# Kernel optimization log

Measured on AMD Instinct MI355X. Metric: run time of the kernel, lower is better.

Reference implementation:

```python
import jax, jax.numpy as jnp
import numpy as np

B, TQ, M, D, H, F, L = 4, 512, 512, 1024, 16, 4096, 6
S = D // H
R = TQ + M  # relative-attention length = memory + query
CUTOFFS = [20000, 40000, 200000]
PROJ_FACTOR = 4
LN_EPS = 1e-6
NEG_INF = -1e9


def setup_inputs() -> dict:
    key = jax.random.key(0)
    ks = iter(jax.random.split(key, 64))

    def w(shape, scale=0.02):
        return jax.random.normal(next(ks), shape, jnp.float32) * scale

    inp = {}
    inp['token_ids'] = jax.random.randint(next(ks), (B, TQ), 0, CUTOFFS[-1])
    inp['memories'] = w((L, B, M, D))
    starts = [0] + CUTOFFS
    pf = 1
    for i in range(len(CUTOFFS)):
        psize = max(1, D // pf)
        inp['emb_table%d' % i] = w((starts[i + 1] - starts[i], psize))
        inp['emb_proj%d' % i] = w((psize, D))
        pf *= PROJ_FACTOR
    inp['wq'] = w((L, D, H, S)); inp['wk'] = w((L, D, H, S))
    inp['wv'] = w((L, D, H, S)); inp['wr'] = w((L, D, H, S))
    inp['wo'] = w((L, H, S, D))
    inp['content_bias'] = w((L, H, S)); inp['position_bias'] = w((L, H, S))
    inp['ln1_scale'] = jnp.ones((L, D)); inp['ln1_bias'] = jnp.zeros((L, D))
    inp['ln2_scale'] = jnp.ones((L, D)); inp['ln2_bias'] = jnp.zeros((L, D))
    inp['ffn_w1'] = w((L, D, F)); inp['ffn_b1'] = jnp.zeros((L, F))
    inp['ffn_w2'] = w((L, F, D)); inp['ffn_b2'] = jnp.zeros((L, D))
    return inp


def layernorm(x, scale, bias):
    mu = jnp.mean(x, axis=-1, keepdims=True)
    var = jnp.var(x, axis=-1, keepdims=True)
    return (x - mu) * jax.lax.rsqrt(var + LN_EPS) * scale + bias


def rel_shift(x):
    # x: [B, H, Q, R] -> shifted so position j aligns with relative distance
    b, h, q, r = x.shape
    x = jnp.pad(x, ((0, 0), (0, 0), (0, 0), (1, 0)))
    x = x.reshape(b, h, r + 1, q)[:, :, 1:, :]
    return x.reshape(b, h, q, r)


def positional_encoding(r_len, d):
    pos = jnp.arange(r_len - 1, -1, -1, dtype=jnp.float32)  # r_len-1 ... 0
    inv_freq = 1.0 / (10000.0 ** (jnp.arange(0, d, 2, dtype=jnp.float32) / d))
    sinusoid = pos[:, None] * inv_freq[None, :]
    return jnp.concatenate([jnp.sin(sinusoid), jnp.cos(sinusoid)], axis=-1)


def adaptive_embed(ids, tables, projs):
    # jit-friendly version of AdaptiveEmbedding.compute_embeddings:
    # gather per-cluster, project up to D, combine via masks.
    d = projs[0].shape[-1]
    y = jnp.zeros(ids.shape + (d,), jnp.float32)
    starts = [0] + CUTOFFS
    for tab, proj, lo, hi in zip(tables, projs, starts[:-1], starts[1:]):
        mask = (ids >= lo) & (ids < hi)
        idx = jnp.clip(ids - lo, 0, tab.shape[0] - 1)
        emb = jnp.einsum('btp,pd->btd', tab[idx], proj)
        y = y + jnp.where(mask[..., None], emb, 0.0)
    return y * (d ** 0.5)


def transformer_xl(token_ids, memories, emb_tables, emb_projs, wq, wk, wv, wr,
                   wo, content_bias, position_bias, ln1_scale, ln1_bias,
                   ln2_scale, ln2_bias, ffn_w1, ffn_b1, ffn_w2, ffn_b2):
    x = adaptive_embed(token_ids, emb_tables, emb_projs)  # [B, TQ, D]
    pe = positional_encoding(R, D)                        # [R, D]
    q_idx = jnp.arange(TQ)[:, None]
    r_idx = jnp.arange(R)[None, :]
    future = r_idx > q_idx + M                            # [TQ, R], True=masked
    scale = 1.0 / np.sqrt(S).astype(np.float32)
    for l in range(L):
        q = jnp.einsum('btd,dhs->bths', x, wq[l])
        kv_in = jnp.concatenate([memories[l], x], axis=1)  # [B, R, D]
        k = jnp.einsum('brd,dhs->brhs', kv_in, wk[l])
        v = jnp.einsum('brd,dhs->brhs', kv_in, wv[l])
        r = jnp.einsum('rd,dhs->rhs', pe, wr[l])
        ac = jnp.einsum('bqhs,brhs->bhqr', q + content_bias[l], k)
        bd = rel_shift(jnp.einsum('bqhs,rhs->bhqr', q + position_bias[l], r))
        scores = (ac + bd) * scale
        scores = jnp.where(future[None, None], NEG_INF, scores)
        attn = jax.nn.softmax(scores, axis=-1)
        ctx = jnp.einsum('bhqr,brhs->bqhs', attn, v)
        out = jnp.einsum('bqhs,hsd->bqd', ctx, wo[l])
        x = layernorm(x + out, ln1_scale[l], ln1_bias[l])
        h = jax.nn.relu(jnp.einsum('btd,df->btf', x, ffn_w1[l]) + ffn_b1[l])
        h = jnp.einsum('btf,fd->btd', h, ffn_w2[l]) + ffn_b2[l]
        x = layernorm(x + h, ln2_scale[l], ln2_bias[l])
    return x


def reference(token_ids, memories, emb_table0, emb_proj0, emb_table1,
              emb_proj1, emb_table2, emb_proj2, wq, wk, wv, wr, wo,
              content_bias, position_bias, ln1_scale, ln1_bias, ln2_scale,
              ln2_bias, ffn_w1, ffn_b1, ffn_w2, ffn_b2):
    return transformer_xl(
        token_ids, memories,
        [emb_table0, emb_table1, emb_table2],
        [emb_proj0, emb_proj1, emb_proj2],
        wq, wk, wv, wr, wo, content_bias, position_bias,
        ln1_scale, ln1_bias, ln2_scale, ln2_bias,
        ffn_w1, ffn_b1, ffn_w2, ffn_b2)
```

## Files before the change

### kernel.cpp

```cpp
#include <hip/hip_runtime.h>


#define Bc 4
#define TQc 512
#define Mc 512
#define Dc 1024
#define Hc 16
#define Sc 64
#define Fc 4096
#define Lc 6
#define Rc 1024
#define KCAT 1344
#define DDc ((size_t)Dc * Dc)
#define NEG_INF_F (-1e9f)

typedef unsigned short ushortT;
typedef __attribute__((ext_vector_type(8))) short bfrag;
typedef __attribute__((ext_vector_type(4))) float facc;

__device__ inline ushortT f2bf(float f) {
    unsigned int u = __builtin_bit_cast(unsigned int, f);
    u = (u + 0x7FFFu + ((u >> 16) & 1u)) >> 16;
    return (ushortT)u;
}

#define CP16(gp, lp)                                                        \
    __builtin_amdgcn_global_load_lds(                                       \
        (const __attribute__((address_space(1))) unsigned int*)(gp),        \
        (__attribute__((address_space(3))) unsigned int*)(lp), 16, 0, 0)

__device__ inline bfrag lds_frag(const ushortT* lds, int row, int cg) {
    int c = cg ^ (row & 7);
    return *reinterpret_cast<const bfrag*>(
        reinterpret_cast<const char*>(lds) + row * 128 + c * 16);
}

template<int BM, int BN, int OUTM, bool BIAS, bool RELU, bool DUALQ,
         bool KVSRC = false, bool KVOUT = false>
__global__ __launch_bounds__(256) void mgemm(
    const ushortT* __restrict__ A, const ushortT* __restrict__ A2,
    const ushortT* __restrict__ Bt,
    const float* __restrict__ bias, const float* __restrict__ bias2,
    float* __restrict__ Cf, ushortT* __restrict__ Cb, ushortT* __restrict__ Cb2,
    int K, int lda, int ldb, int ldc,
    long long sA1, long long sB1, long long sC1, float oscale) {
    constexpr int WTM = BM / 2, WTN = BN / 2;
    constexpr int FM = WTM / 16, FN = WTN / 16;
    __shared__ ushortT sA[2][BM * 64];
    __shared__ ushortT sB[2][BN * 64];
    int tid = threadIdx.x;
    int wave = tid >> 6, lane = tid & 63;
    int r16 = lane & 15, kgrp = lane >> 4;
    int wr = wave >> 1, wc = wave & 1;
    int z = blockIdx.z;
    A  += (long long)z * sA1;
    Bt += (long long)z * sB1;
    long long coff = (long long)z * sC1;
    if (OUTM != 1) Cf += coff;
    if (OUTM != 0 || DUALQ) Cb += coff;

    int row0 = blockIdx.y * BM, col0 = blockIdx.x * BN;
    facc acc[FM][FN] = {};

    auto STAGE = [&](int buf, int k0) {
        #pragma unroll
        for (int it = 0; it < BM / 32; ++it) {
            int s = it * 256 + tid;
            int row = s >> 3, c = s & 7;
            int cs = c ^ (row & 7);
            const char* g;
            if constexpr (KVSRC) {
                int arow = row0 + row;
                int bq = arow >> 10;
                int r = arow & 1023;
                if (r < Mc)
                    g = (const char*)(A + ((size_t)bq * Mc + r) * lda + k0) + cs * 16;
                else
                    g = (const char*)(A2 + ((size_t)bq * TQc + (r - Mc)) * lda + k0) + cs * 16;
            } else {
                g = (const char*)(A + (size_t)(row0 + row) * lda + k0) + cs * 16;
            }
            CP16(g, (char*)sA[buf] + s * 16);
        }
        #pragma unroll
        for (int it = 0; it < BN / 32; ++it) {
            int s = it * 256 + tid;
            int row = s >> 3, c = s & 7;
            int cs = c ^ (row & 7);
            CP16((const char*)(Bt + (size_t)(col0 + row) * ldb + k0) + cs * 16,
                 (char*)sB[buf] + s * 16);
        }
    };

    STAGE(0, 0);
    __syncthreads();
    int nk = K >> 6;
    for (int t = 0; t < nk; ++t) {
        int cur = t & 1;
        if (t + 1 < nk) STAGE(cur ^ 1, (t + 1) << 6);
        #pragma unroll
        for (int ks = 0; ks < 2; ++ks) {
            bfrag af[FM], bf[FN];
            #pragma unroll
            for (int mi = 0; mi < FM; ++mi)
                af[mi] = lds_frag(sA[cur], wr * WTM + mi * 16 + r16, ks * 4 + kgrp);
            #pragma unroll
            for (int ni = 0; ni < FN; ++ni)
                bf[ni] = lds_frag(sB[cur], wc * WTN + ni * 16 + r16, ks * 4 + kgrp);
            #pragma unroll
            for (int mi = 0; mi < FM; ++mi)
                #pragma unroll
                for (int ni = 0; ni < FN; ++ni)
                    acc[mi][ni] = __builtin_amdgcn_mfma_f32_16x16x32_bf16(
                        af[mi], bf[ni], acc[mi][ni], 0, 0, 0);
        }
        __syncthreads();
    }

    if constexpr (KVOUT) {
        if (col0 >= 1024) {
            ushortT* sT = (ushortT*)sA;
            int b = row0 >> 10, r0l = row0 & 1023;
            int h0 = (col0 - 1024) >> 6;
            #pragma unroll
            for (int p = 0; p < 2; ++p) {
                __syncthreads();
                if (wc == p) {
                    #pragma unroll
                    for (int mi = 0; mi < FM; ++mi)
                        #pragma unroll
                        for (int ni = 0; ni < FN; ++ni) {
                            int srow = ni * 16 + r16;
                            int cbase = wr * 64 + mi * 16 + kgrp * 4;
                            short4 s4;
                            s4.x = (short)f2bf(acc[mi][ni][0]);
                            s4.y = (short)f2bf(acc[mi][ni][1]);
                            s4.z = (short)f2bf(acc[mi][ni][2]);
                            s4.w = (short)f2bf(acc[mi][ni][3]);
                            *(short4*)(sT + srow * 132 + cbase) = s4;
                        }
                }
                __syncthreads();
                int h = h0 + p;
                #pragma unroll
                for (int it = 0; it < 4; ++it) {
                    int srow = it * 16 + (tid >> 4);
                    int rch = (tid & 15) * 8;
                    short4 lo = *(short4*)(sT + srow * 132 + rch);
                    short4 hi = *(short4*)(sT + srow * 132 + rch + 4);
                    ushortT* dst = Cb2 + ((size_t)((b * 16 + h) * 64 + srow)) * Rc
                                   + r0l + rch;
                    *(short4*)dst = lo;
                    *(short4*)(dst + 4) = hi;
                }
            }
            return;
        }
    }

    #pragma unroll
    for (int mi = 0; mi < FM; ++mi) {
        #pragma unroll
        for (int ni = 0; ni < FN; ++ni) {
            int gcol = col0 + wc * WTN + ni * 16 + r16;
            float bv = 0.0f, bv2 = 0.0f;
            if (BIAS || DUALQ) bv = bias[gcol];
            if (DUALQ) bv2 = bias2[gcol];
            #pragma unroll
            for (int j = 0; j < 4; ++j) {
                int grow = row0 + wr * WTM + mi * 16 + kgrp * 4 + j;
                float v = acc[mi][ni][j];
                if constexpr (DUALQ) {
                    Cb [(size_t)grow * ldc + gcol] = f2bf((v + bv) * oscale);
                    Cb2[(size_t)grow * ldc + gcol] = f2bf((v + bv2) * oscale);
                } else if constexpr (OUTM == 2) {
                    v *= oscale;
                    Cf[(size_t)grow * ldc + gcol] = v;
                    Cb[(size_t)grow * ldc + gcol] = f2bf(v);
                } else {
                    if (BIAS) v += bv;
                    if (RELU) v = fmaxf(v, 0.0f);
                    if constexpr (OUTM == 0)
                        Cf[(size_t)grow * ldc + gcol] = v;
                    else
                        Cb[(size_t)grow * ldc + gcol] = f2bf(v);
                }
            }
        }
    }
}

__global__ __launch_bounds__(256) void fused_attn(
    const ushortT* __restrict__ qc, const ushortT* __restrict__ qp,
    const ushortT* __restrict__ kb, const ushortT* __restrict__ vT,
    const ushortT* __restrict__ rp, ushortT* __restrict__ ctx) {
    int n_id = (int)(blockIdx.y << 3) | (int)blockIdx.x;
    int b0 = n_id & 1, b7 = (n_id >> 7) & 1, b8 = (n_id >> 8) & 1;
    int u = (b7 << 1) | b0;
    int qt = (b0 ^ b8) ? (7 - u) : u;
    int bh = (n_id >> 1) & 63;
    int b = bh >> 4, h = bh & 15;
    int q0 = qt * 64;
    __shared__ __align__(16) char smem[73728];
    ushortT* sQc = (ushortT*)smem;
    ushortT* sQp = (ushortT*)(smem + 8192);
    float*   sBD = (float*)smem;
    ushortT* sK  = (ushortT*)(smem + 16384);
    ushortT* sV  = (ushortT*)(smem + 32768);
    ushortT* sR  = (ushortT*)(smem + 49152);
    int tid = threadIdx.x;
    int lane = tid & 63, wq = tid >> 6;
    int r16 = lane & 15, kgrp = lane >> 4;
    char* sPb = smem + wq * 4096;

    const ushortT* qcb = qc + (size_t)(b * TQc + q0) * Dc + h * 64;
    const ushortT* qpb = qp + (size_t)(b * TQc + q0) * Dc + h * 64;
    const ushortT* kbb = kb + (size_t)b * Rc * 1024 + h * 64;
    const ushortT* vTb = vT + (size_t)bh * 64 * Rc;
    const ushortT* rpb = rp + h * 64;
    int rrbase0 = 448 - q0;
    int iters = qt + 9;

    #pragma unroll
    for (int it = 0; it < 2; ++it) {
        int s = it * 256 + tid;
        int row = s >> 3, c = s & 7;
        int cs = c ^ (row & 7);
        CP16((const char*)(qcb + (size_t)row * Dc) + cs * 16, (char*)sQc + s * 16);
        CP16((const char*)(qpb + (size_t)row * Dc) + cs * 16, (char*)sQp + s * 16);
        CP16((const char*)(kbb + (size_t)row * 1024) + cs * 16, (char*)sK + s * 16);
        CP16((const char*)(vTb + (size_t)row * Rc) + cs * 16, (char*)sV + s * 16);
    }
    #pragma unroll
    for (int hR = 0; hR < 2; ++hR) {
        #pragma unroll
        for (int it = 0; it < 2; ++it) {
            int s = it * 256 + tid;
            int row = s >> 3, c = s & 7;
            int cs = c ^ (row & 7);
            int gr = rrbase0 + hR * 64 + row;
            gr = gr > 1023 ? 1023 : gr;
            CP16((const char*)(rpb + (size_t)gr * Dc) + cs * 16,
                 (char*)sR + hR * 8192 + s * 16);
        }
    }
    __syncthreads();

    bfrag hqc[2], hqp[2];
    #pragma unroll
    for (int ks = 0; ks < 2; ++ks) {
        hqc[ks] = lds_frag(sQc, wq * 16 + r16, ks * 4 + kgrp);
        hqp[ks] = lds_frag(sQp, wq * 16 + r16, ks * 4 + kgrp);
    }
    __syncthreads();

    facc accO[4] = {};
    float m[4] = {-1e30f, -1e30f, -1e30f, -1e30f};
    float lsum[4] = {};

    for (int itj = 0; itj < iters; ++itj) {
        int j0 = itj * 64;
        __syncthreads();
        int cur = itj & 1;
        int ph0 = itj % 3, ph1 = (itj + 1) % 3;

        if (itj + 1 < iters) {
            int jn = j0 + 64;
            #pragma unroll
            for (int it2 = 0; it2 < 2; ++it2) {
                int s = it2 * 256 + tid;
                int row = s >> 3, c = s & 7;
                int cs = c ^ (row & 7);
                CP16((const char*)(kbb + (size_t)(jn + row) * 1024) + cs * 16,
                     (char*)sK + (cur ^ 1) * 8192 + s * 16);
                CP16((const char*)(vTb + (size_t)row * Rc + jn) + cs * 16,
                     (char*)sV + (cur ^ 1) * 8192 + s * 16);
            }
        }
        if (itj + 2 <= iters) {
            int L = itj + 2;
            int p2 = L % 3;
            #pragma unroll
            for (int it2 = 0; it2 < 2; ++it2) {
                int s = it2 * 256 + tid;
                int row = s >> 3, c = s & 7;
                int cs = c ^ (row & 7);
                int gr = rrbase0 + L * 64 + row;
                gr = gr > 1023 ? 1023 : gr;
                CP16((const char*)(rpb + (size_t)gr * Dc) + cs * 16,
                     (char*)sR + p2 * 8192 + s * 16);
            }
        }

        facc aac[4] = {};
        facc abd[5] = {};
        __builtin_amdgcn_s_setprio(1);
        #pragma unroll
        for (int ks = 0; ks < 2; ++ks) {
            #pragma unroll
            for (int n = 0; n < 4; ++n) {
                bfrag bk = lds_frag(sK + cur * 4096, n * 16 + r16, ks * 4 + kgrp);
                aac[n] = __builtin_amdgcn_mfma_f32_16x16x32_bf16(hqc[ks], bk, aac[n], 0, 0, 0);
            }
            #pragma unroll
            for (int n = 0; n < 5; ++n) {
                int t = 3 - wq + n;
                int p = (t >> 2) ? ph1 : ph0;
                bfrag br = lds_frag(sR + p * 4096, (t & 3) * 16 + r16, ks * 4 + kgrp);
                abd[n] = __builtin_amdgcn_mfma_f32_16x16x32_bf16(hqp[ks], br, abd[n], 0, 0, 0);
            }
        }
        __builtin_amdgcn_s_setprio(0);
        #pragma unroll
        for (int n = 0; n < 5; ++n) {
            int rl = (3 - wq + n) * 16 + r16;
            #pragma unroll
            for (int jj = 0; jj < 4; ++jj) {
                int ql = wq * 16 + kgrp * 4 + jj;
                int jl = rl + ql - 63;
                if (jl >= 0 && jl < 64)
                    sBD[ql * 64 + (jl ^ (((ql >> 2) & 1) << 4))] = abd[n][jj];
            }
        }

        bool lastit = (itj == iters - 1);
        float P[4][4];
        #pragma unroll
        for (int jj = 0; jj < 4; ++jj) {
            int ql = wq * 16 + kgrp * 4 + jj;
            int swz = ((ql >> 2) & 1) << 4;
            float sv[4];
            #pragma unroll
            for (int n = 0; n < 4; ++n) {
                int jl = n * 16 + r16;
                sv[n] = aac[n][jj] + sBD[ql * 64 + (jl ^ swz)];
            }
            if (lastit) {
                int qg = q0 + ql;
                #pragma unroll
                for (int n = 0; n < 4; ++n) {
                    int jg = j0 + n * 16 + r16;
                    if (jg > qg + Mc) sv[n] = NEG_INF_F;
                }
            }
            float mx = fmaxf(fmaxf(sv[0], sv[1]), fmaxf(sv[2], sv[3]));
            mx = fmaxf(mx, __shfl_xor(mx, 1));
            mx = fmaxf(mx, __shfl_xor(mx, 2));
            mx = fmaxf(mx, __shfl_xor(mx, 4));
            mx = fmaxf(mx, __shfl_xor(mx, 8));
            float mnew = fmaxf(m[jj], mx);
            float corr = __expf(m[jj] - mnew);
            m[jj] = mnew;
            float rs = 0.0f;
            #pragma unroll
            for (int n = 0; n < 4; ++n) {
                float p = __expf(sv[n] - mnew);
                P[n][jj] = p;
                rs += p;
            }
            rs += __shfl_xor(rs, 1);
            rs += __shfl_xor(rs, 2);
            rs += __shfl_xor(rs, 4);
            rs += __shfl_xor(rs, 8);
            lsum[jj] = lsum[jj] * corr + rs;
            #pragma unroll
            for (int n = 0; n < 4; ++n) accO[n][jj] *= corr;
        }
        #pragma unroll
        for (int jj = 0; jj < 4; ++jj) {
            int row = wq * 16 + kgrp * 4 + jj;
            #pragma unroll
            for (int n = 0; n < 4; ++n) {
                int col = n * 16 + r16;
                int boff = (row & 15) * 128 + (((col >> 3) ^ (row & 7)) * 16) + (col & 7) * 2;
                *(ushortT*)(sPb + boff) = f2bf(P[n][jj]);
            }
        }
        __builtin_amdgcn_s_setprio(1);
        #pragma unroll
        for (int ks = 0; ks < 2; ++ks) {
            bfrag pa = *(const bfrag*)(sPb + r16 * 128 + (((ks * 4 + kgrp) ^ (r16 & 7)) * 16));
            #pragma unroll
            for (int n = 0; n < 4; ++n) {
                bfrag bv = lds_frag(sV + cur * 4096, n * 16 + r16, ks * 4 + kgrp);
                accO[n] = __builtin_amdgcn_mfma_f32_16x16x32_bf16(pa, bv, accO[n], 0, 0, 0);
            }
        }
        __builtin_amdgcn_s_setprio(0);
    }
    #pragma unroll
    for (int jj = 0; jj < 4; ++jj) {
        int qg = q0 + wq * 16 + kgrp * 4 + jj;
        float inv = 1.0f / lsum[jj];
        #pragma unroll
        for (int n = 0; n < 4; ++n) {
            int col = n * 16 + r16;
            ctx[(size_t)(b * TQc + qg) * Dc + h * 64 + col] = f2bf(accO[n][jj] * inv);
        }
    }
}

__global__ __launch_bounds__(256) void tr_f32_bf16(
    const float* __restrict__ in, ushortT* __restrict__ out, int R0, int C0,
    int ldout, int coff, long long inZ, long long outZ) {
    in += (long long)blockIdx.z * inZ;
    out += (long long)blockIdx.z * outZ;
    __shared__ float t[32][33];
    int tx = threadIdx.x & 31, ty = threadIdx.x >> 5;
    int c0 = blockIdx.x * 32, r0 = blockIdx.y * 32;
    #pragma unroll
    for (int i = 0; i < 4; ++i)
        t[ty + i * 8][tx] = in[(size_t)(r0 + ty + i * 8) * C0 + c0 + tx];
    __syncthreads();
    int c = threadIdx.x >> 3, rq = (threadIdx.x & 7) << 2;
    short4 s4;
    s4.x = (short)f2bf(t[rq + 0][c]);
    s4.y = (short)f2bf(t[rq + 1][c]);
    s4.z = (short)f2bf(t[rq + 2][c]);
    s4.w = (short)f2bf(t[rq + 3][c]);
    *(short4*)(out + (size_t)(c0 + c) * ldout + coff + r0 + rq) = s4;
}

__global__ __launch_bounds__(256) void tr_dxd5(
    const float* __restrict__ wr, const float* __restrict__ wq,
    const float* __restrict__ wk, const float* __restrict__ wv,
    const float* __restrict__ wo,
    ushortT* __restrict__ wrT, ushortT* __restrict__ wqT,
    ushortT* __restrict__ wkvT, ushortT* __restrict__ woT) {
    int sel = blockIdx.z / Lc, l = blockIdx.z % Lc;
    const float* in; ushortT* out;
    if (sel == 0)      { in = wr + l * DDc; out = wrT + l * DDc; }
    else if (sel == 1) { in = wq + l * DDc; out = wqT + l * DDc; }
    else if (sel == 2) { in = wk + l * DDc; out = wkvT + l * 2 * DDc; }
    else if (sel == 3) { in = wv + l * DDc; out = wkvT + l * 2 * DDc + DDc; }
    else               { in = wo + l * DDc; out = woT + l * DDc; }
    __shared__ float t[32][33];
    int tx = threadIdx.x & 31, ty = threadIdx.x >> 5;
    int c0 = blockIdx.x * 32, r0 = blockIdx.y * 32;
    #pragma unroll
    for (int i = 0; i < 4; ++i)
        t[ty + i * 8][tx] = in[(size_t)(r0 + ty + i * 8) * Dc + c0 + tx];
    __syncthreads();
    int c = threadIdx.x >> 3, rq = (threadIdx.x & 7) << 2;
    short4 s4;
    s4.x = (short)f2bf(t[rq + 0][c]);
    s4.y = (short)f2bf(t[rq + 1][c]);
    s4.z = (short)f2bf(t[rq + 2][c]);
    s4.w = (short)f2bf(t[rq + 3][c]);
    *(short4*)(out + (size_t)(c0 + c) * Dc + r0 + rq) = s4;
}

__global__ __launch_bounds__(256) void pos_enc_kernel(ushortT* __restrict__ pe) {
    int idx = blockIdx.x * 256 + threadIdx.x;
    int r = idx >> 10;
    int d = idx & 1023;
    float pos = (float)(Rc - 1 - r);
    int i = (d < 512) ? d : (d - 512);
    float inv_freq = 1.0f / powf(10000.0f, (2.0f * (float)i) / 1024.0f);
    float arg = pos * inv_freq;
    pe[idx] = f2bf((d < 512) ? sinf(arg) : cosf(arg));
}

__global__ __launch_bounds__(256) void gather_embed(
    const int* __restrict__ ids,
    const float* __restrict__ t0, const float* __restrict__ t1,
    const float* __restrict__ t2, ushortT* __restrict__ gcat) {
    int token = blockIdx.x;
    int id = ids[token];
    ushortT* row = gcat + (size_t)token * KCAT;
    short4 z4 = {0, 0, 0, 0};
    for (int t = threadIdx.x; t < KCAT / 4; t += 256)
        reinterpret_cast<short4*>(row)[t] = z4;
    __syncthreads();
    const float* tab; int psize, lo, o;
    if (id < 20000)      { tab = t0; psize = 1024; lo = 0;     o = 0; }
    else if (id < 40000) { tab = t1; psize = 256;  lo = 20000; o = 1024; }
    else                 { tab = t2; psize = 64;   lo = 40000; o = 1280; }
    const float* src = tab + (size_t)(id - lo) * psize;
    for (int p4 = threadIdx.x; p4 < psize / 4; p4 += 256) {
        float4 v = reinterpret_cast<const float4*>(src)[p4];
        short4 s4;
        s4.x = (short)f2bf(v.x); s4.y = (short)f2bf(v.y);
        s4.z = (short)f2bf(v.z); s4.w = (short)f2bf(v.w);
        reinterpret_cast<short4*>(row + o)[p4] = s4;
    }
}

__global__ __launch_bounds__(256) void cast_f32_bf16(
    const float* __restrict__ in, ushortT* __restrict__ o) {
    size_t i8 = ((size_t)blockIdx.x * 256 + threadIdx.x) * 8;
    const float4* m4 = (const float4*)(in + i8);
    float4 a = m4[0], c = m4[1];
    int4 p;
    p.x = (int)f2bf(a.x) | ((int)f2bf(a.y) << 16);
    p.y = (int)f2bf(a.z) | ((int)f2bf(a.w) << 16);
    p.z = (int)f2bf(c.x) | ((int)f2bf(c.y) << 16);
    p.w = (int)f2bf(c.z) | ((int)f2bf(c.w) << 16);
    *(int4*)(o + i8) = p;
}

template<int NP, bool CBIAS>
__global__ __launch_bounds__(256) void add_ln_kernel(
    const float* __restrict__ xin, const float* __restrict__ r0,
    const float* __restrict__ r1, const float* __restrict__ r2,
    const float* __restrict__ r3, const float* __restrict__ cbias,
    const float* __restrict__ scale, const float* __restrict__ bias,
    float* __restrict__ dst, ushortT* __restrict__ dstb) {
    int row = blockIdx.x * 4 + (threadIdx.x >> 6);
    int lane = threadIdx.x & 63;
    const float4* xr = (const float4*)(xin + (size_t)row * Dc);
    const float4* p0 = (const float4*)(r0 + (size_t)row * Dc);
    const float4* p1 = nullptr; const float4* p2 = nullptr; const float4* p3 = nullptr;
    if constexpr (NP > 1) p1 = (const float4*)(r1 + (size_t)row * Dc);
    if constexpr (NP > 2) p2 = (const float4*)(r2 + (size_t)row * Dc);
    if constexpr (NP > 3) p3 = (const float4*)(r3 + (size_t)row * Dc);
    const float4* cb4 = CBIAS ? (const float4*)cbias : nullptr;
    float4 v[4];
    float s = 0.0f, s2 = 0.0f;
    #pragma unroll
    for (int rep = 0; rep < 4; ++rep) {
        int idx = rep * 64 + lane;
        float4 a = xr[idx];
        float4 b = p0[idx];
        a.x += b.x; a.y += b.y; a.z += b.z; a.w += b.w;
        if constexpr (NP > 1) {
            float4 c1 = p1[idx];
            a.x += c1.x; a.y += c1.y; a.z += c1.z; a.w += c1.w;
        }
        if constexpr (NP > 2) {
            float4 c2 = p2[idx];
            a.x += c2.x; a.y += c2.y; a.z += c2.z; a.w += c2.w;
        }
        if constexpr (NP > 3) {
            float4 c3 = p3[idx];
            a.x += c3.x; a.y += c3.y; a.z += c3.z; a.w += c3.w;
        }
        if constexpr (CBIAS) {
            float4 cbv = cb4[idx];
            a.x += cbv.x; a.y += cbv.y; a.z += cbv.z; a.w += cbv.w;
        }
        v[rep] = a;
        s += a.x + a.y + a.z + a.w;
        s2 += a.x * a.x + a.y * a.y + a.z * a.z + a.w * a.w;
    }
    #pragma unroll
    for (int o = 1; o < 64; o <<= 1) {
        s += __shfl_xor(s, o);
        s2 += __shfl_xor(s2, o);
    }
    float mean = s * (1.0f / Dc);
    float var = s2 * (1.0f / Dc) - mean * mean;
    float rstd = rsqrtf(var + 1e-6f);
    float4* d4 = (float4*)(dst + (size_t)row * Dc);
    short4* db4 = (short4*)(dstb + (size_t)row * Dc);
    const float4* sc4 = (const float4*)scale;
    const float4* bi4 = (const float4*)bias;
    #pragma unroll
    for (int rep = 0; rep < 4; ++rep) {
        int idx = rep * 64 + lane;
        float4 scv = sc4[idx], biv = bi4[idx];
        float4 a = v[rep];
        float4 o;
        o.x = (a.x - mean) * rstd * scv.x + biv.x;
        o.y = (a.y - mean) * rstd * scv.y + biv.y;
        o.z = (a.z - mean) * rstd * scv.z + biv.z;
        o.w = (a.w - mean) * rstd * scv.w + biv.w;
        d4[idx] = o;
        short4 ob;
        ob.x = (short)f2bf(o.x); ob.y = (short)f2bf(o.y);
        ob.z = (short)f2bf(o.z); ob.w = (short)f2bf(o.w);
        db4[idx] = ob;
    }
}

extern "C" void kernel_launch(void* const* d_in, const int* in_sizes, int n_in,
                              void* d_out, int out_size, void* d_ws, size_t ws_size,
                              hipStream_t stream) {
    const int*   token_ids = (const int*)d_in[0];
    const float* memories  = (const float*)d_in[1];
    const float* tab0 = (const float*)d_in[2];
    const float* prj0 = (const float*)d_in[3];
    const float* tab1 = (const float*)d_in[4];
    const float* prj1 = (const float*)d_in[5];
    const float* tab2 = (const float*)d_in[6];
    const float* prj2 = (const float*)d_in[7];
    const float* wq = (const float*)d_in[8];
    const float* wk = (const float*)d_in[9];
    const float* wv = (const float*)d_in[10];
    const float* wr = (const float*)d_in[11];
    const float* wo = (const float*)d_in[12];
    const float* cb = (const float*)d_in[13];
    const float* pb = (const float*)d_in[14];
    const float* ln1s = (const float*)d_in[15];
    const float* ln1b = (const float*)d_in[16];
    const float* ln2s = (const float*)d_in[17];
    const float* ln2b = (const float*)d_in[18];
    const float* w1 = (const float*)d_in[19];
    const float* b1 = (const float*)d_in[20];
    const float* w2 = (const float*)d_in[21];
    const float* b2 = (const float*)d_in[22];
    float* out = (float*)d_out;

    char* wsb = (char*)d_ws;
    size_t off = 0;
    auto alloc = [&](size_t bytes) {
        char* p = wsb + off;
        off += (bytes + 255) & ~(size_t)255;
        return p;
    };
    const size_t DD = DDc;
    const size_t TD = (size_t)Bc * TQc * Dc;
    const size_t DF = (size_t)Dc * Fc;
    ushortT* pe_b  = (ushortT*)alloc((size_t)Rc * Dc * 2);
    ushortT* wrT   = (ushortT*)alloc((size_t)Lc * DD * 2);
    ushortT* rpA   = (ushortT*)alloc((size_t)Lc * Rc * Dc * 2);
    ushortT* wqT   = (ushortT*)alloc((size_t)Lc * DD * 2);
    ushortT* wkvT  = (ushortT*)alloc((size_t)Lc * 2 * DD * 2);
    ushortT* woT   = (ushortT*)alloc((size_t)Lc * DD * 2);
    ushortT* w1T   = (ushortT*)alloc((size_t)Lc * DF * 2);
    ushortT* w2T   = (ushortT*)alloc((size_t)Lc * DF * 2);
    ushortT* memb  = (ushortT*)alloc((size_t)Lc * Bc * Mc * Dc * 2);
    ushortT* gcat  = (ushortT*)alloc((size_t)Bc * TQc * KCAT * 2);
    ushortT* WcatT = (ushortT*)alloc((size_t)Dc * KCAT * 2);
    float*   x     = (float*)alloc(TD * 4);
    ushortT* xb    = (ushortT*)alloc(TD * 2);
    ushortT* qc    = (ushortT*)alloc(TD * 2);
    ushortT* qp    = (ushortT*)alloc(TD * 2);
    ushortT* kbuf  = (ushortT*)alloc((size_t)Bc * Rc * 1024 * 2);
    ushortT* vT    = (ushortT*)alloc((size_t)Bc * Rc * Dc * 2);
    ushortT* ctxb  = (ushortT*)alloc(TD * 2);
    float*   obp   = (float*)alloc(4 * TD * 4);
    ushortT* hb    = (ushortT*)alloc((size_t)Bc * TQc * Fc * 2);

    pos_enc_kernel<<<(Rc * Dc) / 256, 256, 0, stream>>>(pe_b);
    gather_embed<<<Bc * TQc, 256, 0, stream>>>(token_ids, tab0, tab1, tab2, gcat);
    tr_f32_bf16<<<dim3(32, 32), 256, 0, stream>>>(prj0, WcatT, 1024, 1024, KCAT, 0, 0, 0);
    tr_f32_bf16<<<dim3(32, 8), 256, 0, stream>>>(prj1, WcatT, 256, 1024, KCAT, 1024, 0, 0);
    tr_f32_bf16<<<dim3(32, 2), 256, 0, stream>>>(prj2, WcatT, 64, 1024, KCAT, 1280, 0, 0);
    mgemm<64, 64, 2, false, false, false><<<dim3(16, 32), 256, 0, stream>>>(
        gcat, nullptr, WcatT, nullptr, nullptr, x, xb, nullptr,
        KCAT, KCAT, KCAT, Dc, 0, 0, 0, 32.0f);

    tr_dxd5<<<dim3(32, 32, 5 * Lc), 256, 0, stream>>>(
        wr, wq, wk, wv, wo, wrT, wqT, wkvT, woT);
    tr_f32_bf16<<<dim3(128, 32, Lc), 256, 0, stream>>>(w1, w1T, Dc, Fc, Dc, 0, DF, DF);
    tr_f32_bf16<<<dim3(32, 128, Lc), 256, 0, stream>>>(w2, w2T, Fc, Dc, Fc, 0, DF, DF);
    cast_f32_bf16<<<(Lc * Bc * Mc * Dc) / (256 * 8), 256, 0, stream>>>(memories, memb);
    mgemm<64, 64, 1, false, false, false><<<dim3(16, 16, Lc), 256, 0, stream>>>(
        pe_b, nullptr, wrT, nullptr, nullptr, nullptr, rpA, nullptr,
        Dc, Dc, Dc, Dc, 0, (long long)DD, (long long)Rc * Dc, 1.0f);

    for (int l = 0; l < Lc; ++l) {
        const ushortT* membl = memb + (size_t)l * Bc * Mc * Dc;
        mgemm<64, 64, 1, false, false, true><<<dim3(16, 32), 256, 0, stream>>>(
            xb, nullptr, wqT + (size_t)l * DD, cb + (size_t)l * Dc, pb + (size_t)l * Dc,
            nullptr, qc, qp, Dc, Dc, Dc, Dc, 0, 0, 0, 0.125f);
        mgemm<128, 128, 1, false, false, false, true, true>
            <<<dim3(16, 32), 256, 0, stream>>>(
            membl, xb, wkvT + (size_t)l * 2 * DD, nullptr, nullptr,
            nullptr, kbuf, vT, Dc, Dc, Dc, 1024, 0, 0, 0, 1.0f);

        fused_attn<<<dim3(8, 64), 256, 0, stream>>>(
            qc, qp, kbuf, vT, rpA + (size_t)l * Rc * Dc, ctxb);

        mgemm<64, 64, 0, false, false, false><<<dim3(16, 32), 256, 0, stream>>>(
            ctxb, nullptr, woT + (size_t)l * DD, nullptr, nullptr, obp, nullptr, nullptr,
            Dc, Dc, Dc, Dc, 0, 0, 0, 1.0f);
        add_ln_kernel<1, false><<<Bc * TQc / 4, 256, 0, stream>>>(
            x, obp, nullptr, nullptr, nullptr, nullptr,
            ln1s + (size_t)l * Dc, ln1b + (size_t)l * Dc, x, xb);
        mgemm<128, 128, 1, true, true, false><<<dim3(32, 16), 256, 0, stream>>>(
            xb, nullptr, w1T + (size_t)l * DF, b1 + (size_t)l * Fc, nullptr,
            nullptr, hb, nullptr, Dc, Dc, Dc, Fc, 0, 0, 0, 1.0f);
        mgemm<128, 128, 0, false, false, false><<<dim3(8, 16, 4), 256, 0, stream>>>(
            hb, nullptr, w2T + (size_t)l * DF, nullptr, nullptr, obp, nullptr, nullptr,
            1024, Fc, Fc, Dc, 1024, 1024, (long long)TD, 1.0f);
        add_ln_kernel<4, true><<<Bc * TQc / 4, 256, 0, stream>>>(
            x, obp, obp + TD, obp + 2 * TD, obp + 3 * TD, b2 + (size_t)l * Dc,
            ln2s + (size_t)l * Dc, ln2b + (size_t)l * Dc,
            (l == Lc - 1) ? out : x, xb);
    }
}
```

Baseline: 1.259 ms.

## Merge Q and KV projection launches; reduce FFN2 split-K via atomics

Q-projection and K/V-projection GEMMs now run in one launch, with blockIdx.z choosing which tile body to execute over shared LDS. The FFN2 split-K GEMM now accumulates its four partial results into one fp32 buffer with atomic adds instead of writing four separate partials. That buffer is zeroed inside the first add+layernorm kernel, and the second layernorm reads a single partial. This cuts one launch per layer and the memory traffic of the extra partial buffers, at the cost of atomic contention and a fixed 128x128-sized LDS allocation for the smaller Q tiles.

```diff
diff --git a/kernel.cpp b/kernel.cpp
--- a/kernel.cpp
+++ b/kernel.cpp
@@ -37,29 +37,23 @@
 
 template<int BM, int BN, int OUTM, bool BIAS, bool RELU, bool DUALQ,
          bool KVSRC = false, bool KVOUT = false>
-__global__ __launch_bounds__(256) void mgemm(
+__device__ __forceinline__ void mgemm_body(
+    char* smemraw,
     const ushortT* __restrict__ A, const ushortT* __restrict__ A2,
     const ushortT* __restrict__ Bt,
     const float* __restrict__ bias, const float* __restrict__ bias2,
     float* __restrict__ Cf, ushortT* __restrict__ Cb, ushortT* __restrict__ Cb2,
-    int K, int lda, int ldb, int ldc,
-    long long sA1, long long sB1, long long sC1, float oscale) {
+    int K, int lda, int ldb, int ldc, float oscale, int bx, int by) {
     constexpr int WTM = BM / 2, WTN = BN / 2;
     constexpr int FM = WTM / 16, FN = WTN / 16;
-    __shared__ ushortT sA[2][BM * 64];
-    __shared__ ushortT sB[2][BN * 64];
+    ushortT* sAb = (ushortT*)smemraw;
+    ushortT* sBb = sAb + 2 * BM * 64;
     int tid = threadIdx.x;
     int wave = tid >> 6, lane = tid & 63;
     int r16 = lane & 15, kgrp = lane >> 4;
     int wr = wave >> 1, wc = wave & 1;
-    int z = blockIdx.z;
-    A  += (long long)z * sA1;
-    Bt += (long long)z * sB1;
-    long long coff = (long long)z * sC1;
-    if (OUTM != 1) Cf += coff;
-    if (OUTM != 0 || DUALQ) Cb += coff;
-
-    int row0 = blockIdx.y * BM, col0 = blockIdx.x * BN;
+
+    int row0 = by * BM, col0 = bx * BN;
     facc acc[FM][FN] = {};
 
     auto STAGE = [&](int buf, int k0) {
@@ -80,7 +74,7 @@
             } else {
                 g = (const char*)(A + (size_t)(row0 + row) * lda + k0) + cs * 16;
             }
-            CP16(g, (char*)sA[buf] + s * 16);
+            CP16(g, (char*)(sAb + buf * BM * 64) + s * 16);
         }
         #pragma unroll
         for (int it = 0; it < BN / 32; ++it) {
@@ -88,7 +82,7 @@
             int row = s >> 3, c = s & 7;
             int cs = c ^ (row & 7);
             CP16((const char*)(Bt + (size_t)(col0 + row) * ldb + k0) + cs * 16,
-                 (char*)sB[buf] + s * 16);
+                 (char*)(sBb + buf * BN * 64) + s * 16);
         }
     };
 
@@ -103,10 +97,10 @@
             bfrag af[FM], bf[FN];
             #pragma unroll
             for (int mi = 0; mi < FM; ++mi)
-                af[mi] = lds_frag(sA[cur], wr * WTM + mi * 16 + r16, ks * 4 + kgrp);
+                af[mi] = lds_frag(sAb + cur * BM * 64, wr * WTM + mi * 16 + r16, ks * 4 + kgrp);
             #pragma unroll
             for (int ni = 0; ni < FN; ++ni)
-                bf[ni] = lds_frag(sB[cur], wc * WTN + ni * 16 + r16, ks * 4 + kgrp);
+                bf[ni] = lds_frag(sBb + cur * BN * 64, wc * WTN + ni * 16 + r16, ks * 4 + kgrp);
             #pragma unroll
             for (int mi = 0; mi < FM; ++mi)
                 #pragma unroll
@@ -119,7 +113,7 @@
 
     if constexpr (KVOUT) {
         if (col0 >= 1024) {
-            ushortT* sT = (ushortT*)sA;
+            ushortT* sT = sAb;
             int b = row0 >> 10, r0l = row0 & 1023;
             int h0 = (col0 - 1024) >> 6;
             #pragma unroll
@@ -182,12 +176,52 @@
                     if (RELU) v = fmaxf(v, 0.0f);
                     if constexpr (OUTM == 0)
                         Cf[(size_t)grow * ldc + gcol] = v;
+                    else if constexpr (OUTM == 3)
+                        unsafeAtomicAdd(&Cf[(size_t)grow * ldc + gcol], v);
                     else
                         Cb[(size_t)grow * ldc + gcol] = f2bf(v);
                 }
             }
         }
     }
+}
+
+template<int BM, int BN, int OUTM, bool BIAS, bool RELU, bool DUALQ,
+         bool KVSRC = false, bool KVOUT = false>
+__global__ __launch_bounds__(256) void mgemm(
+    const ushortT* __restrict__ A, const ushortT* __restrict__ A2,
+    const ushortT* __restrict__ Bt,
+    const float* __restrict__ bias, const float* __restrict__ bias2,
+    float* __restrict__ Cf, ushortT* __restrict__ Cb, ushortT* __restrict__ Cb2,
+    int K, int lda, int ldb, int ldc,
+    long long sA1, long long sB1, long long sC1, float oscale) {
+    __shared__ char smem[2 * (BM + BN) * 64 * 2];
+    int z = blockIdx.z;
+    A  += (long long)z * sA1;
+    Bt += (long long)z * sB1;
+    long long coff = (long long)z * sC1;
+    if (OUTM != 1) Cf += coff;
+    if (OUTM != 0 || DUALQ) Cb += coff;
+    mgemm_body<BM, BN, OUTM, BIAS, RELU, DUALQ, KVSRC, KVOUT>(
+        smem, A, A2, Bt, bias, bias2, Cf, Cb, Cb2,
+        K, lda, ldb, ldc, oscale, blockIdx.x, blockIdx.y);
+}
+
+__global__ __launch_bounds__(256) void qkv_gemm(
+    const ushortT* __restrict__ xb, const ushortT* __restrict__ membl,
+    const ushortT* __restrict__ wqTl, const ushortT* __restrict__ wkvTl,
+    const float* __restrict__ cbl, const float* __restrict__ pbl,
+    ushortT* __restrict__ qc, ushortT* __restrict__ qp,
+    ushortT* __restrict__ kbuf, ushortT* __restrict__ vT) {
+    __shared__ char smem[2 * (128 + 128) * 64 * 2];
+    if (blockIdx.z == 0)
+        mgemm_body<64, 64, 1, false, false, true, false, false>(
+            smem, xb, nullptr, wqTl, cbl, pbl, nullptr, qc, qp,
+            Dc, Dc, Dc, Dc, 0.125f, blockIdx.x, blockIdx.y);
+    else
+        mgemm_body<128, 128, 1, false, false, false, true, true>(
+            smem, membl, xb, wkvTl, nullptr, nullptr, nullptr, kbuf, vT,
+            Dc, Dc, Dc, 1024, 1.0f, blockIdx.x, blockIdx.y);
 }
 
 __global__ __launch_bounds__(256) void fused_attn(
@@ -499,13 +533,14 @@
     *(int4*)(o + i8) = p;
 }
 
-template<int NP, bool CBIAS>
+template<int NP, bool CBIAS, bool ZR0 = false>
 __global__ __launch_bounds__(256) void add_ln_kernel(
     const float* __restrict__ xin, const float* __restrict__ r0,
     const float* __restrict__ r1, const float* __restrict__ r2,
     const float* __restrict__ r3, const float* __restrict__ cbias,
     const float* __restrict__ scale, const float* __restrict__ bias,
-    float* __restrict__ dst, ushortT* __restrict__ dstb) {
+    float* __restrict__ dst, ushortT* __restrict__ dstb,
+    float* __restrict__ r0z) {
     int row = blockIdx.x * 4 + (threadIdx.x >> 6);
     int lane = threadIdx.x & 63;
     const float4* xr = (const float4*)(xin + (size_t)row * Dc);
@@ -542,6 +577,12 @@
         v[rep] = a;
         s += a.x + a.y + a.z + a.w;
         s2 += a.x * a.x + a.y * a.y + a.z * a.z + a.w * a.w;
+    }
+    if constexpr (ZR0) {
+        float4 zz = {0.0f, 0.0f, 0.0f, 0.0f};
+        float4* z4 = (float4*)(r0z + (size_t)row * Dc);
+        #pragma unroll
+        for (int rep = 0; rep < 4; ++rep) z4[rep * 64 + lane] = zz;
     }
     #pragma unroll
     for (int o = 1; o < 64; o <<= 1) {
@@ -629,7 +670,7 @@
     ushortT* kbuf  = (ushortT*)alloc((size_t)Bc * Rc * 1024 * 2);
     ushortT* vT    = (ushortT*)alloc((size_t)Bc * Rc * Dc * 2);
     ushortT* ctxb  = (ushortT*)alloc(TD * 2);
-    float*   obp   = (float*)alloc(4 * TD * 4);
+    float*   obp   = (float*)alloc(TD * 4);
     ushortT* hb    = (ushortT*)alloc((size_t)Bc * TQc * Fc * 2);
 
     pos_enc_kernel<<<(Rc * Dc) / 256, 256, 0, stream>>>(pe_b);
@@ -652,13 +693,9 @@
 
     for (int l = 0; l < Lc; ++l) {
         const ushortT* membl = memb + (size_t)l * Bc * Mc * Dc;
-        mgemm<64, 64, 1, false, false, true><<<dim3(16, 32), 256, 0, stream>>>(
-            xb, nullptr, wqT + (size_t)l * DD, cb + (size_t)l * Dc, pb + (size_t)l * Dc,
-            nullptr, qc, qp, Dc, Dc, Dc, Dc, 0, 0, 0, 0.125f);
-        mgemm<128, 128, 1, false, false, false, true, true>
-            <<<dim3(16, 32), 256, 0, stream>>>(
-            membl, xb, wkvT + (size_t)l * 2 * DD, nullptr, nullptr,
-            nullptr, kbuf, vT, Dc, Dc, Dc, 1024, 0, 0, 0, 1.0f);
+        qkv_gemm<<<dim3(16, 32, 2), 256, 0, stream>>>(
+            xb, membl, wqT + (size_t)l * DD, wkvT + (size_t)l * 2 * DD,
+            cb + (size_t)l * Dc, pb + (size_t)l * Dc, qc, qp, kbuf, vT);
 
         fused_attn<<<dim3(8, 64), 256, 0, stream>>>(
             qc, qp, kbuf, vT, rpA + (size_t)l * Rc * Dc, ctxb);
@@ -666,18 +703,18 @@
         mgemm<64, 64, 0, false, false, false><<<dim3(16, 32), 256, 0, stream>>>(
             ctxb, nullptr, woT + (size_t)l * DD, nullptr, nullptr, obp, nullptr, nullptr,
             Dc, Dc, Dc, Dc, 0, 0, 0, 1.0f);
-        add_ln_kernel<1, false><<<Bc * TQc / 4, 256, 0, stream>>>(
+        add_ln_kernel<1, false, true><<<Bc * TQc / 4, 256, 0, stream>>>(
             x, obp, nullptr, nullptr, nullptr, nullptr,
-            ln1s + (size_t)l * Dc, ln1b + (size_t)l * Dc, x, xb);
+            ln1s + (size_t)l * Dc, ln1b + (size_t)l * Dc, x, xb, obp);
         mgemm<128, 128, 1, true, true, false><<<dim3(32, 16), 256, 0, stream>>>(
             xb, nullptr, w1T + (size_t)l * DF, b1 + (size_t)l * Fc, nullptr,
             nullptr, hb, nullptr, Dc, Dc, Dc, Fc, 0, 0, 0, 1.0f);
-        mgemm<128, 128, 0, false, false, false><<<dim3(8, 16, 4), 256, 0, stream>>>(
+        mgemm<128, 128, 3, false, false, false><<<dim3(8, 16, 4), 256, 0, stream>>>(
             hb, nullptr, w2T + (size_t)l * DF, nullptr, nullptr, obp, nullptr, nullptr,
-            1024, Fc, Fc, Dc, 1024, 1024, (long long)TD, 1.0f);
-        add_ln_kernel<4, true><<<Bc * TQc / 4, 256, 0, stream>>>(
-            x, obp, obp + TD, obp + 2 * TD, obp + 3 * TD, b2 + (size_t)l * Dc,
+            1024, Fc, Fc, Dc, 1024, 1024, 0, 1.0f);
+        add_ln_kernel<1, true, false><<<Bc * TQc / 4, 256, 0, stream>>>(
+            x, obp, nullptr, nullptr, nullptr, b2 + (size_t)l * Dc,
             ln2s + (size_t)l * Dc, ln2b + (size_t)l * Dc,
-            (l == Lc - 1) ? out : x, xb);
-    }
-}
+            (l == Lc - 1) ? out : x, xb, nullptr);
+    }
+}
```

Result: no change. 1.249 ms (-0.8%).
